# Optimization experiments

Hardware: AMD Instinct MI355X
Metric: run time of the kernel (lower is better)

## Reference

```python
import jax, jax.numpy as jnp
import numpy as np

BINS = 10
LOSS_WEIGHT = 1.0


def setup_inputs() -> dict:
    key = jax.random.key(0)
    k1, k2 = jax.random.split(key)
    N, C = 32768, 1024
    pred = jax.random.normal(k1, (N, C), dtype=jnp.float32)
    target = jax.random.randint(k2, (N,), 0, C, dtype=jnp.int32)
    return {"pred": pred, "target": target}


def reference(pred, target):
    N, C = pred.shape
    # one-hot target (torch scatter_ of 1 at label index)
    t = jax.nn.one_hot(target, C, dtype=pred.dtype)  # [N, C]
    # gradient norm g = |sigmoid(pred).detach() - target|, in [0, 1]
    g = jnp.abs(jax.nn.sigmoid(jax.lax.stop_gradient(pred)) - t)
    # all samples valid (label_weight=None -> ones); tot = max(sum(valid), 1)
    tot = jnp.asarray(N * C, dtype=pred.dtype)
    # edges = arange(bins+1)/bins with edges[-1] += 1e-6: bin = floor(g*bins),
    # g == 1.0 falls in last bin -> clip to bins-1
    bin_idx = jnp.clip((g * BINS).astype(jnp.int32), 0, BINS - 1)  # [N, C]
    counts = jnp.bincount(bin_idx.ravel(), length=BINS).astype(pred.dtype)  # [BINS]
    nonempty = counts > 0
    n = jnp.maximum(jnp.sum(nonempty).astype(pred.dtype), 1.0)
    # per-bin weight tot/num_in_bin for nonempty bins, then divide by n
    w_bin = jnp.where(nonempty, tot / jnp.maximum(counts, 1.0), 0.0) / n
    weights = w_bin[bin_idx]  # gather back to [N, C]
    # stable BCE-with-logits, weighted, reduction='sum'
    bce = jnp.maximum(pred, 0.0) - pred * t + jnp.log1p(jnp.exp(-jnp.abs(pred)))
    loss = jnp.sum(weights * bce) / tot
    return loss * LOSS_WEIGHT
```

## Files before the change

kernel.cpp:

```cpp
#include <hip/hip_runtime.h>
#include <math.h>


#define PASS1_BLOCK 256
#define PASS1_GRID 2048

typedef float v2f __attribute__((ext_vector_type(2)));
typedef float v4f __attribute__((ext_vector_type(4)));

__device__ __forceinline__ void wave_red(float& v) {
#pragma unroll
    for (int off = 32; off > 0; off >>= 1) v += __shfl_down(v, off, 64);
}

__device__ __constant__ float kThresh[9] = {
    -2.1972246f, -1.3862944f, -0.84729786f, -0.40546511f, 0.0f,
    0.40546511f, 0.84729786f, 1.3862944f, 2.1972246f};

__device__ __forceinline__ void upd(float p, float& S0, v2f (&A)[9]) {
    float a = fabsf(p);
    float en = __expf(-a);
    float l1p = __logf(1.0f + en);
    float bce = fmaxf(p, 0.0f) + l1p;
    S0 += bce;
    v2f bv = {bce, 1.0f};
#pragma unroll
    for (int q = 0; q < 9; ++q) {
        float m = (p >= kThresh[q]) ? 1.0f : 0.0f;
        v2f mv = {m, m};
        A[q] += bv * mv;
    }
}

__device__ __forceinline__ void upd_corr(float p, float& S0, v2f (&A)[9]) {
    float a = fabsf(p);
    float en = __expf(-a);
    float l1p = __logf(1.0f + en);
    float bf = fmaxf(p, 0.0f) + l1p;
    float bt = fmaxf(-p, 0.0f) + l1p;
    S0 += bt - bf;
#pragma unroll
    for (int q = 0; q < 9; ++q) {
        float mf = (p >= kThresh[q]) ? 1.0f : 0.0f;
        float mt = (-p >= kThresh[q]) ? 1.0f : 0.0f;
        v2f d = {mt * bt - mf * bf, mt - mf};
        A[q] += d;
    }
}

__global__ __launch_bounds__(PASS1_BLOCK, 8) void ghmc_pass1(
    const float* __restrict__ pred, const int* __restrict__ target,
    float* __restrict__ blk, unsigned total4, unsigned totalNC, int N, int C) {
    float S0 = 0.0f;
    v2f A[9];
#pragma unroll
    for (int i = 0; i < 9; ++i) A[i] = (v2f){0.0f, 0.0f};

    unsigned tid = blockIdx.x * blockDim.x + threadIdx.x;
    unsigned stride = gridDim.x * blockDim.x;
    const v4f* p4 = (const v4f*)pred;

    for (unsigned v = tid; v < total4; v += stride) {
        v4f p = __builtin_nontemporal_load(p4 + v);
        upd(p[0], S0, A);
        upd(p[1], S0, A);
        upd(p[2], S0, A);
        upd(p[3], S0, A);
    }

    if (tid == 0) {
        for (unsigned e = total4 << 2; e < totalNC; ++e) upd(pred[e], S0, A);
    }

    int row = (int)(blockIdx.x * blockDim.x + threadIdx.x);
    if (row < N) {
        int t = target[row];
        float p = pred[(unsigned)row * (unsigned)C + (unsigned)t];
        upd_corr(p, S0, A);
    }

    float vals[19];
    vals[0] = S0;
#pragma unroll
    for (int i = 0; i < 9; ++i) {
        vals[1 + i] = A[i].x;
        vals[10 + i] = A[i].y;
    }
#pragma unroll
    for (int i = 0; i < 19; ++i) wave_red(vals[i]);

    __shared__ float sP[PASS1_BLOCK / 64][19];
    int wid = threadIdx.x >> 6;
    int lane = threadIdx.x & 63;
    if (lane == 0) {
#pragma unroll
        for (int i = 0; i < 19; ++i) sP[wid][i] = vals[i];
    }
    __syncthreads();
    if (threadIdx.x == 0) {
        const int nw = PASS1_BLOCK / 64;
#pragma unroll
        for (int i = 0; i < 19; ++i) {
            float acc = 0.0f;
            for (int w = 0; w < nw; ++w) acc += sP[w][i];
            blk[(unsigned)blockIdx.x * 19u + (unsigned)i] = acc;
        }
    }
}

__global__ __launch_bounds__(256) void ghmc_pass2(
    const float* __restrict__ blk, float* __restrict__ out, int nblocks,
    float totalNC) {
    float P[19];
#pragma unroll
    for (int i = 0; i < 19; ++i) P[i] = 0.0f;

    for (int b = threadIdx.x; b < nblocks; b += blockDim.x) {
#pragma unroll
        for (int i = 0; i < 19; ++i) P[i] += blk[(unsigned)b * 19u + (unsigned)i];
    }
#pragma unroll
    for (int i = 0; i < 19; ++i) wave_red(P[i]);

    __shared__ float sP[4][19];
    int wid = threadIdx.x >> 6;
    int lane = threadIdx.x & 63;
    if (lane == 0) {
#pragma unroll
        for (int i = 0; i < 19; ++i) sP[wid][i] = P[i];
    }
    __syncthreads();
    if (threadIdx.x == 0) {
        float Sv[11], Cv[11];
        for (int i = 0; i < 19; ++i) {
            float a = 0.0f;
            for (int w = 0; w < 4; ++w) a += sP[w][i];
            P[i] = a;
        }
        for (int i = 0; i < 10; ++i) Sv[i] = P[i];
        Sv[10] = 0.0f;
        Cv[0] = totalNC;
        for (int i = 1; i < 10; ++i) Cv[i] = P[9 + i];
        Cv[10] = 0.0f;

        int nonempty = 0;
        for (int b = 0; b < 10; ++b)
            if (Cv[b] - Cv[b + 1] > 0.5f) nonempty++;
        float n = fmaxf((float)nonempty, 1.0f);

        float loss = 0.0f;
        for (int b = 0; b < 10; ++b) {
            float cnt = Cv[b] - Cv[b + 1];
            if (cnt > 0.5f) {
                float bs = Sv[b] - Sv[b + 1];
                loss += bs / (cnt * n);
            }
        }
        out[0] = loss;
    }
}

extern "C" void kernel_launch(void* const* d_in, const int* in_sizes, int n_in,
                              void* d_out, int out_size, void* d_ws, size_t ws_size,
                              hipStream_t stream) {
    const float* pred = (const float*)d_in[0];
    const int* target = (const int*)d_in[1];
    int NC = in_sizes[0];
    int N = in_sizes[1];
    int C = NC / N;
    unsigned total4 = (unsigned)(NC / 4);

    int blocks = PASS1_GRID;
    size_t per_block = 19 * sizeof(float);
    if (ws_size < (size_t)blocks * per_block) {
        size_t maxb = ws_size / per_block;
        blocks = (int)(maxb > 0 ? maxb : 1);
    }

    float* blkbuf = (float*)d_ws;

    ghmc_pass1<<<blocks, PASS1_BLOCK, 0, stream>>>(pred, target, blkbuf, total4,
                                                   (unsigned)NC, N, C);
    ghmc_pass2<<<1, 256, 0, stream>>>(blkbuf, (float*)d_out, blocks, (float)NC);
}
```

Before: 218.5 us.

## Fuse reduction passes with atomics and count bins via wave ballot popcount

Merges the two-kernel reduction into one kernel. Each block atomically adds its partial sums and counts into global accumulators, and the last block, detected with a ticket counter, computes the final loss. Per-element bin counts move from float vector accumulation to integer wave ballot plus popcount, which cuts per-thread VALU work for counts. It adds a memset launch, global atomics and fence overhead, and makes float summation order nondeterministic.

```diff
diff --git a/kernel.cpp b/kernel.cpp
--- a/kernel.cpp
+++ b/kernel.cpp
@@ -2,59 +2,57 @@
 #include <math.h>
 
 
-#define PASS1_BLOCK 256
-#define PASS1_GRID 2048
+#define BLK 256
+#define GRID 2048
 
-typedef float v2f __attribute__((ext_vector_type(2)));
 typedef float v4f __attribute__((ext_vector_type(4)));
+
+__device__ __constant__ float kT[9] = {
+    -2.1972246f, -1.3862944f, -0.84729786f, -0.40546511f, 0.0f,
+    0.40546511f, 0.84729786f, 1.3862944f, 2.1972246f};
 
 __device__ __forceinline__ void wave_red(float& v) {
 #pragma unroll
     for (int off = 32; off > 0; off >>= 1) v += __shfl_down(v, off, 64);
 }
 
-__device__ __constant__ float kThresh[9] = {
-    -2.1972246f, -1.3862944f, -0.84729786f, -0.40546511f, 0.0f,
-    0.40546511f, 0.84729786f, 1.3862944f, 2.1972246f};
-
-__device__ __forceinline__ void upd(float p, float& S0, v2f (&A)[9]) {
-    float a = fabsf(p);
-    float en = __expf(-a);
-    float l1p = __logf(1.0f + en);
-    float bce = fmaxf(p, 0.0f) + l1p;
-    S0 += bce;
-    v2f bv = {bce, 1.0f};
+__device__ __forceinline__ void upd(float x, float (&S)[10], int (&cnt)[9]) {
+    float en = __expf(-fabsf(x));
+    float bce = fmaxf(x, 0.0f) + __logf(1.0f + en);
+    S[0] += bce;
 #pragma unroll
     for (int q = 0; q < 9; ++q) {
-        float m = (p >= kThresh[q]) ? 1.0f : 0.0f;
-        v2f mv = {m, m};
-        A[q] += bv * mv;
+        bool b = (x >= kT[q]);
+        S[q + 1] += b ? bce : 0.0f;
+        cnt[q] += (int)__popcll(__ballot(b));
     }
 }
 
-__device__ __forceinline__ void upd_corr(float p, float& S0, v2f (&A)[9]) {
-    float a = fabsf(p);
-    float en = __expf(-a);
+__device__ __forceinline__ void upd_corr(float p, float (&S)[10], int (&cnt)[9]) {
+    float en = __expf(-fabsf(p));
     float l1p = __logf(1.0f + en);
     float bf = fmaxf(p, 0.0f) + l1p;
     float bt = fmaxf(-p, 0.0f) + l1p;
-    S0 += bt - bf;
+    S[0] += bt - bf;
 #pragma unroll
     for (int q = 0; q < 9; ++q) {
-        float mf = (p >= kThresh[q]) ? 1.0f : 0.0f;
-        float mt = (-p >= kThresh[q]) ? 1.0f : 0.0f;
-        v2f d = {mt * bt - mf * bf, mt - mf};
-        A[q] += d;
+        bool btq = (-p >= kT[q]);
+        bool bfq = (p >= kT[q]);
+        S[q + 1] += (btq ? bt : 0.0f) - (bfq ? bf : 0.0f);
+        cnt[q] += (int)__popcll(__ballot(btq)) - (int)__popcll(__ballot(bfq));
     }
 }
 
-__global__ __launch_bounds__(PASS1_BLOCK, 8) void ghmc_pass1(
+__global__ __launch_bounds__(BLK, 8) void ghmc_fused(
     const float* __restrict__ pred, const int* __restrict__ target,
-    float* __restrict__ blk, unsigned total4, unsigned totalNC, int N, int C) {
-    float S0 = 0.0f;
-    v2f A[9];
+    float* __restrict__ gS, int* __restrict__ gC, unsigned* __restrict__ gT,
+    float* __restrict__ out, unsigned total4, unsigned totalNC, int N, int C) {
+    float S[10];
+    int cnt[9];
 #pragma unroll
-    for (int i = 0; i < 9; ++i) A[i] = (v2f){0.0f, 0.0f};
+    for (int i = 0; i < 10; ++i) S[i] = 0.0f;
+#pragma unroll
+    for (int i = 0; i < 9; ++i) cnt[i] = 0;
 
     unsigned tid = blockIdx.x * blockDim.x + threadIdx.x;
     unsigned stride = gridDim.x * blockDim.x;
@@ -62,101 +60,75 @@
 
     for (unsigned v = tid; v < total4; v += stride) {
         v4f p = __builtin_nontemporal_load(p4 + v);
-        upd(p[0], S0, A);
-        upd(p[1], S0, A);
-        upd(p[2], S0, A);
-        upd(p[3], S0, A);
+        upd(p[0], S, cnt);
+        upd(p[1], S, cnt);
+        upd(p[2], S, cnt);
+        upd(p[3], S, cnt);
     }
 
     if (tid == 0) {
-        for (unsigned e = total4 << 2; e < totalNC; ++e) upd(pred[e], S0, A);
+        for (unsigned e = total4 << 2; e < totalNC; ++e) upd(pred[e], S, cnt);
     }
 
-    int row = (int)(blockIdx.x * blockDim.x + threadIdx.x);
+    int row = (int)tid;
     if (row < N) {
         int t = target[row];
         float p = pred[(unsigned)row * (unsigned)C + (unsigned)t];
-        upd_corr(p, S0, A);
+        upd_corr(p, S, cnt);
     }
 
-    float vals[19];
-    vals[0] = S0;
 #pragma unroll
-    for (int i = 0; i < 9; ++i) {
-        vals[1 + i] = A[i].x;
-        vals[10 + i] = A[i].y;
-    }
-#pragma unroll
-    for (int i = 0; i < 19; ++i) wave_red(vals[i]);
+    for (int i = 0; i < 10; ++i) wave_red(S[i]);
 
-    __shared__ float sP[PASS1_BLOCK / 64][19];
+    __shared__ float sS[BLK / 64][10];
+    __shared__ int sC[BLK / 64][9];
     int wid = threadIdx.x >> 6;
     int lane = threadIdx.x & 63;
     if (lane == 0) {
 #pragma unroll
-        for (int i = 0; i < 19; ++i) sP[wid][i] = vals[i];
+        for (int i = 0; i < 10; ++i) sS[wid][i] = S[i];
+#pragma unroll
+        for (int i = 0; i < 9; ++i) sC[wid][i] = cnt[i];
     }
     __syncthreads();
+
     if (threadIdx.x == 0) {
-        const int nw = PASS1_BLOCK / 64;
+        const int nw = BLK / 64;
 #pragma unroll
-        for (int i = 0; i < 19; ++i) {
-            float acc = 0.0f;
-            for (int w = 0; w < nw; ++w) acc += sP[w][i];
-            blk[(unsigned)blockIdx.x * 19u + (unsigned)i] = acc;
+        for (int i = 0; i < 10; ++i) {
+            float a = 0.0f;
+            for (int w = 0; w < nw; ++w) a += sS[w][i];
+            atomicAdd(&gS[i], a);
         }
-    }
-}
+#pragma unroll
+        for (int i = 0; i < 9; ++i) {
+            int a = 0;
+            for (int w = 0; w < nw; ++w) a += sC[w][i];
+            atomicAdd(&gC[i], a);
+        }
+        __threadfence();
+        unsigned old = atomicAdd(gT, 1u);
+        if (old == gridDim.x - 1u) {
+            __threadfence();
+            float Sv[11], Cv[11];
+            for (int i = 0; i < 10; ++i) Sv[i] = atomicAdd(&gS[i], 0.0f);
+            Sv[10] = 0.0f;
+            Cv[0] = (float)totalNC;
+            for (int i = 1; i < 10; ++i) Cv[i] = (float)atomicAdd(&gC[i - 1], 0);
+            Cv[10] = 0.0f;
 
-__global__ __launch_bounds__(256) void ghmc_pass2(
-    const float* __restrict__ blk, float* __restrict__ out, int nblocks,
-    float totalNC) {
-    float P[19];
-#pragma unroll
-    for (int i = 0; i < 19; ++i) P[i] = 0.0f;
+            int nonempty = 0;
+            for (int b = 0; b < 10; ++b)
+                if (Cv[b] - Cv[b + 1] > 0.5f) nonempty++;
+            float n = fmaxf((float)nonempty, 1.0f);
 
-    for (int b = threadIdx.x; b < nblocks; b += blockDim.x) {
-#pragma unroll
-        for (int i = 0; i < 19; ++i) P[i] += blk[(unsigned)b * 19u + (unsigned)i];
-    }
-#pragma unroll
-    for (int i = 0; i < 19; ++i) wave_red(P[i]);
-
-    __shared__ float sP[4][19];
-    int wid = threadIdx.x >> 6;
-    int lane = threadIdx.x & 63;
-    if (lane == 0) {
-#pragma unroll
-        for (int i = 0; i < 19; ++i) sP[wid][i] = P[i];
-    }
-    __syncthreads();
-    if (threadIdx.x == 0) {
-        float Sv[11], Cv[11];
-        for (int i = 0; i < 19; ++i) {
-            float a = 0.0f;
-            for (int w = 0; w < 4; ++w) a += sP[w][i];
-            P[i] = a;
+            float loss = 0.0f;
+            for (int b = 0; b < 10; ++b) {
+                float c = Cv[b] - Cv[b + 1];
+                if (c > 0.5f) loss += (Sv[b] - Sv[b + 1]) / (c * n);
+            }
+            out[0] = loss;
         }
-        for (int i = 0; i < 10; ++i) Sv[i] = P[i];
-        Sv[10] = 0.0f;
-        Cv[0] = totalNC;
-        for (int i = 1; i < 10; ++i) Cv[i] = P[9 + i];
-        Cv[10] = 0.0f;
-
-        int nonempty = 0;
-        for (int b = 0; b < 10; ++b)
-            if (Cv[b] - Cv[b + 1] > 0.5f) nonempty++;
-        float n = fmaxf((float)nonempty, 1.0f);
-
-        float loss = 0.0f;
-        for (int b = 0; b < 10; ++b) {
-            float cnt = Cv[b] - Cv[b + 1];
-            if (cnt > 0.5f) {
-                float bs = Sv[b] - Sv[b + 1];
-                loss += bs / (cnt * n);
-            }
-        }
-        out[0] = loss;
     }
 }
 
@@ -170,16 +142,13 @@
     int C = NC / N;
     unsigned total4 = (unsigned)(NC / 4);
 
-    int blocks = PASS1_GRID;
-    size_t per_block = 19 * sizeof(float);
-    if (ws_size < (size_t)blocks * per_block) {
-        size_t maxb = ws_size / per_block;
-        blocks = (int)(maxb > 0 ? maxb : 1);
-    }
+    float* gS = (float*)d_ws;
+    int* gC = (int*)((char*)d_ws + 64);
+    unsigned* gT = (unsigned*)((char*)d_ws + 128);
 
-    float* blkbuf = (float*)d_ws;
+    hipMemsetAsync(d_ws, 0, 192, stream);
 
-    ghmc_pass1<<<blocks, PASS1_BLOCK, 0, stream>>>(pred, target, blkbuf, total4,
-                                                   (unsigned)NC, N, C);
-    ghmc_pass2<<<1, 256, 0, stream>>>(blkbuf, (float*)d_out, blocks, (float)NC);
+    ghmc_fused<<<GRID, BLK, 0, stream>>>(pred, target, gS, gC, gT,
+                                         (float*)d_out, total4, (unsigned)NC,
+                                         N, C);
 }
```

Measured after the change: 458.5 us. 110% more time.

## Replace threshold-cumulative accumulation with per-thread LDS histogram bins

Applied to the files above, without the earlier changes.

Before this change, each element was compared against 9 logit thresholds and accumulated into cumulative sum and count registers, with bins recovered by differencing in the final pass. Now each element computes its sigmoid bin directly and does LDS atomics into per-thread, padded histogram slots (10 bins × 257 stride), which removes the 9-way compare-and-accumulate per element. The main loop is also unrolled to two v4 loads per iteration, the nontemporal loads become plain loads, and occupancy drops to 4 blocks per CU. This trades ALU work for two LDS atomics per element plus about 20 KB of shared memory per block, which may lower occupancy.

```diff
diff --git a/kernel.cpp b/kernel.cpp
--- a/kernel.cpp
+++ b/kernel.cpp
@@ -2,10 +2,10 @@
 #include <math.h>
 
 
-#define PASS1_BLOCK 256
-#define PASS1_GRID 2048
+#define BLK 256
+#define GRID 2048
+#define BSTRIDE 257
 
-typedef float v2f __attribute__((ext_vector_type(2)));
 typedef float v4f __attribute__((ext_vector_type(4)));
 
 __device__ __forceinline__ void wave_red(float& v) {
@@ -13,148 +13,160 @@
     for (int off = 32; off > 0; off >>= 1) v += __shfl_down(v, off, 64);
 }
 
-__device__ __constant__ float kThresh[9] = {
-    -2.1972246f, -1.3862944f, -0.84729786f, -0.40546511f, 0.0f,
-    0.40546511f, 0.84729786f, 1.3862944f, 2.1972246f};
+__device__ __forceinline__ void upd(float x, float* __restrict__ sSum,
+                                    int* __restrict__ sCnt, int tid) {
+    float a = fabsf(x);
+    float en = __expf(-a);
+    float den = 1.0f + en;
+    float l1p = __logf(den);
+    float r = __builtin_amdgcn_rcpf(den);
+    float numer = (x >= 0.0f) ? 1.0f : en;
+    float sig = numer * r;
+    int bin = (int)(sig * 10.0f);
+    bin = bin > 9 ? 9 : bin;
+    float bce = fmaxf(x, 0.0f) + l1p;
+    atomicAdd(&sSum[bin * BSTRIDE + tid], bce);
+    atomicAdd(&sCnt[bin * BSTRIDE + tid], 1);
+}
 
-__device__ __forceinline__ void upd(float p, float& S0, v2f (&A)[9]) {
+__device__ __forceinline__ void upd_corr(float p, float* __restrict__ sSum,
+                                         int* __restrict__ sCnt, int tid) {
     float a = fabsf(p);
     float en = __expf(-a);
-    float l1p = __logf(1.0f + en);
-    float bce = fmaxf(p, 0.0f) + l1p;
-    S0 += bce;
-    v2f bv = {bce, 1.0f};
-#pragma unroll
-    for (int q = 0; q < 9; ++q) {
-        float m = (p >= kThresh[q]) ? 1.0f : 0.0f;
-        v2f mv = {m, m};
-        A[q] += bv * mv;
-    }
+    float den = 1.0f + en;
+    float l1p = __logf(den);
+    float r = __builtin_amdgcn_rcpf(den);
+    float numer = (p >= 0.0f) ? 1.0f : en;
+    float sigp = numer * r;
+    float sigt = 1.0f - sigp;
+    int bf = (int)(sigp * 10.0f);
+    bf = bf > 9 ? 9 : bf;
+    int bt = (int)(sigt * 10.0f);
+    bt = bt > 9 ? 9 : bt;
+    float bce_f = fmaxf(p, 0.0f) + l1p;
+    float bce_t = fmaxf(-p, 0.0f) + l1p;
+    atomicAdd(&sSum[bf * BSTRIDE + tid], -bce_f);
+    atomicAdd(&sCnt[bf * BSTRIDE + tid], -1);
+    atomicAdd(&sSum[bt * BSTRIDE + tid], bce_t);
+    atomicAdd(&sCnt[bt * BSTRIDE + tid], 1);
 }
 
-__device__ __forceinline__ void upd_corr(float p, float& S0, v2f (&A)[9]) {
-    float a = fabsf(p);
-    float en = __expf(-a);
-    float l1p = __logf(1.0f + en);
-    float bf = fmaxf(p, 0.0f) + l1p;
-    float bt = fmaxf(-p, 0.0f) + l1p;
-    S0 += bt - bf;
-#pragma unroll
-    for (int q = 0; q < 9; ++q) {
-        float mf = (p >= kThresh[q]) ? 1.0f : 0.0f;
-        float mt = (-p >= kThresh[q]) ? 1.0f : 0.0f;
-        v2f d = {mt * bt - mf * bf, mt - mf};
-        A[q] += d;
-    }
-}
-
-__global__ __launch_bounds__(PASS1_BLOCK, 8) void ghmc_pass1(
+__global__ __launch_bounds__(BLK, 4) void ghmc_pass1(
     const float* __restrict__ pred, const int* __restrict__ target,
     float* __restrict__ blk, unsigned total4, unsigned totalNC, int N, int C) {
-    float S0 = 0.0f;
-    v2f A[9];
-#pragma unroll
-    for (int i = 0; i < 9; ++i) A[i] = (v2f){0.0f, 0.0f};
+    __shared__ float sSum[10 * BSTRIDE];
+    __shared__ int sCnt[10 * BSTRIDE];
 
-    unsigned tid = blockIdx.x * blockDim.x + threadIdx.x;
-    unsigned stride = gridDim.x * blockDim.x;
+    int tid = threadIdx.x;
+    for (int i = tid; i < 10 * BSTRIDE; i += BLK) {
+        sSum[i] = 0.0f;
+        sCnt[i] = 0;
+    }
+    __syncthreads();
+
+    unsigned gtid = blockIdx.x * BLK + tid;
+    unsigned stride = gridDim.x * BLK;
     const v4f* p4 = (const v4f*)pred;
 
-    for (unsigned v = tid; v < total4; v += stride) {
-        v4f p = __builtin_nontemporal_load(p4 + v);
-        upd(p[0], S0, A);
-        upd(p[1], S0, A);
-        upd(p[2], S0, A);
-        upd(p[3], S0, A);
+    unsigned v = gtid;
+    for (; v + stride < total4; v += 2u * stride) {
+        v4f a = p4[v];
+        v4f b = p4[v + stride];
+        upd(a[0], sSum, sCnt, tid);
+        upd(a[1], sSum, sCnt, tid);
+        upd(a[2], sSum, sCnt, tid);
+        upd(a[3], sSum, sCnt, tid);
+        upd(b[0], sSum, sCnt, tid);
+        upd(b[1], sSum, sCnt, tid);
+        upd(b[2], sSum, sCnt, tid);
+        upd(b[3], sSum, sCnt, tid);
+    }
+    for (; v < total4; v += stride) {
+        v4f a = p4[v];
+        upd(a[0], sSum, sCnt, tid);
+        upd(a[1], sSum, sCnt, tid);
+        upd(a[2], sSum, sCnt, tid);
+        upd(a[3], sSum, sCnt, tid);
     }
 
-    if (tid == 0) {
-        for (unsigned e = total4 << 2; e < totalNC; ++e) upd(pred[e], S0, A);
+    if (gtid == 0) {
+        for (unsigned e = total4 << 2; e < totalNC; ++e)
+            upd(pred[e], sSum, sCnt, tid);
     }
 
-    int row = (int)(blockIdx.x * blockDim.x + threadIdx.x);
-    if (row < N) {
-        int t = target[row];
-        float p = pred[(unsigned)row * (unsigned)C + (unsigned)t];
-        upd_corr(p, S0, A);
+    if ((int)gtid < N) {
+        int t = target[gtid];
+        float p = pred[gtid * (unsigned)C + (unsigned)t];
+        upd_corr(p, sSum, sCnt, tid);
     }
 
-    float vals[19];
-    vals[0] = S0;
+    __syncthreads();
+
+    float vals[20];
 #pragma unroll
-    for (int i = 0; i < 9; ++i) {
-        vals[1 + i] = A[i].x;
-        vals[10 + i] = A[i].y;
+    for (int b = 0; b < 10; ++b) {
+        vals[b] = sSum[b * BSTRIDE + tid];
+        vals[10 + b] = (float)sCnt[b * BSTRIDE + tid];
     }
 #pragma unroll
-    for (int i = 0; i < 19; ++i) wave_red(vals[i]);
+    for (int i = 0; i < 20; ++i) wave_red(vals[i]);
 
-    __shared__ float sP[PASS1_BLOCK / 64][19];
-    int wid = threadIdx.x >> 6;
-    int lane = threadIdx.x & 63;
+    __shared__ float sW[BLK / 64][20];
+    int wid = tid >> 6;
+    int lane = tid & 63;
     if (lane == 0) {
 #pragma unroll
-        for (int i = 0; i < 19; ++i) sP[wid][i] = vals[i];
+        for (int i = 0; i < 20; ++i) sW[wid][i] = vals[i];
     }
     __syncthreads();
-    if (threadIdx.x == 0) {
-        const int nw = PASS1_BLOCK / 64;
+    if (tid == 0) {
+        float* dst = blk + (unsigned)blockIdx.x * 20u;
 #pragma unroll
-        for (int i = 0; i < 19; ++i) {
+        for (int i = 0; i < 20; ++i) {
             float acc = 0.0f;
-            for (int w = 0; w < nw; ++w) acc += sP[w][i];
-            blk[(unsigned)blockIdx.x * 19u + (unsigned)i] = acc;
+            for (int w = 0; w < BLK / 64; ++w) acc += sW[w][i];
+            dst[i] = acc;
         }
     }
 }
 
 __global__ __launch_bounds__(256) void ghmc_pass2(
-    const float* __restrict__ blk, float* __restrict__ out, int nblocks,
-    float totalNC) {
-    float P[19];
+    const float* __restrict__ blk, float* __restrict__ out, int nblocks) {
+    float P[20];
 #pragma unroll
-    for (int i = 0; i < 19; ++i) P[i] = 0.0f;
+    for (int i = 0; i < 20; ++i) P[i] = 0.0f;
 
-    for (int b = threadIdx.x; b < nblocks; b += blockDim.x) {
+    for (int b = threadIdx.x; b < nblocks; b += 256) {
+        const float* src = blk + (unsigned)b * 20u;
 #pragma unroll
-        for (int i = 0; i < 19; ++i) P[i] += blk[(unsigned)b * 19u + (unsigned)i];
+        for (int i = 0; i < 20; ++i) P[i] += src[i];
     }
 #pragma unroll
-    for (int i = 0; i < 19; ++i) wave_red(P[i]);
+    for (int i = 0; i < 20; ++i) wave_red(P[i]);
 
-    __shared__ float sP[4][19];
+    __shared__ float sP[4][20];
     int wid = threadIdx.x >> 6;
     int lane = threadIdx.x & 63;
     if (lane == 0) {
 #pragma unroll
-        for (int i = 0; i < 19; ++i) sP[wid][i] = P[i];
+        for (int i = 0; i < 20; ++i) sP[wid][i] = P[i];
     }
     __syncthreads();
     if (threadIdx.x == 0) {
-        float Sv[11], Cv[11];
-        for (int i = 0; i < 19; ++i) {
+#pragma unroll
+        for (int i = 0; i < 20; ++i) {
             float a = 0.0f;
             for (int w = 0; w < 4; ++w) a += sP[w][i];
             P[i] = a;
         }
-        for (int i = 0; i < 10; ++i) Sv[i] = P[i];
-        Sv[10] = 0.0f;
-        Cv[0] = totalNC;
-        for (int i = 1; i < 10; ++i) Cv[i] = P[9 + i];
-        Cv[10] = 0.0f;
-
         int nonempty = 0;
         for (int b = 0; b < 10; ++b)
-            if (Cv[b] - Cv[b + 1] > 0.5f) nonempty++;
+            if (P[10 + b] > 0.5f) nonempty++;
         float n = fmaxf((float)nonempty, 1.0f);
 
         float loss = 0.0f;
         for (int b = 0; b < 10; ++b) {
-            float cnt = Cv[b] - Cv[b + 1];
-            if (cnt > 0.5f) {
-                float bs = Sv[b] - Sv[b + 1];
-                loss += bs / (cnt * n);
-            }
+            if (P[10 + b] > 0.5f) loss += P[b] / (P[10 + b] * n);
         }
         out[0] = loss;
     }
@@ -170,8 +182,8 @@
     int C = NC / N;
     unsigned total4 = (unsigned)(NC / 4);
 
-    int blocks = PASS1_GRID;
-    size_t per_block = 19 * sizeof(float);
+    int blocks = GRID;
+    size_t per_block = 20 * sizeof(float);
     if (ws_size < (size_t)blocks * per_block) {
         size_t maxb = ws_size / per_block;
         blocks = (int)(maxb > 0 ? maxb : 1);
@@ -179,7 +191,7 @@
 
     float* blkbuf = (float*)d_ws;
 
-    ghmc_pass1<<<blocks, PASS1_BLOCK, 0, stream>>>(pred, target, blkbuf, total4,
-                                                   (unsigned)NC, N, C);
-    ghmc_pass2<<<1, 256, 0, stream>>>(blkbuf, (float*)d_out, blocks, (float)NC);
+    ghmc_pass1<<<blocks, BLK, 0, stream>>>(pred, target, blkbuf, total4,
+                                           (unsigned)NC, N, C);
+    ghmc_pass2<<<1, 256, 0, stream>>>(blkbuf, (float*)d_out, blocks);
 }
```

Result: slower. 334.1 us (+52.9%).
